# Kernel tuning notes

Hardware: AMD Instinct MI355X
Metric: run time of the kernel (lower is better)

## Reference

```python
import jax, jax.numpy as jnp
import numpy as np

NUM_CLASSES = 10
NUM_NODES = 4096
BATCH = 2048
T_TRAIN = 2048
WDIM = 64
GAMMA = 1.0
ADJ_P = 0.02  # edge density


def setup_inputs() -> dict:
    key = jax.random.key(0)
    ks = jax.random.split(key, 7)
    pred = jax.random.normal(ks[0], (BATCH, NUM_CLASSES), dtype=jnp.float32)
    target = jax.random.randint(ks[1], (BATCH,), 0, NUM_CLASSES, dtype=jnp.int32)
    mask_idx = jnp.arange(BATCH, dtype=jnp.int32)  # nodes selected by boolean `mask`
    adj = jax.random.bernoulli(ks[2], ADJ_P, (NUM_NODES, NUM_NODES))  # bool adjacency
    gem = jax.random.normal(ks[3], (NUM_NODES, T_TRAIN), dtype=jnp.float32)  # global_effect_matrix[:, train_mask]
    w_sub = jax.random.uniform(ks[4], (WDIM, T_TRAIN), dtype=jnp.float32)
    w_inter = jax.random.uniform(ks[5], (WDIM, T_TRAIN), dtype=jnp.float32)
    w_global = jax.random.uniform(ks[6], (WDIM, T_TRAIN), dtype=jnp.float32)
    return dict(pred=pred, gem=gem, w_sub=w_sub, w_inter=w_inter,
                w_global=w_global, adj=adj, target=target, mask_idx=mask_idx)


def reference(pred, gem, w_sub, w_inter, w_global, adj, target, mask_idx):
    B = pred.shape[0]
    dt = pred.dtype
    # linear_*(gem).sum(-1) == gem @ W.sum(0)
    g_sub = gem @ w_sub.sum(axis=0)      # [Nn]
    g_inter = gem @ w_inter.sum(axis=0)  # [Nn]
    g_global = gem @ w_global.sum(axis=0)  # computed in original (vg_i) but unused by loss

    A = adj[mask_idx].astype(dt)                    # [B, Nn] rows of adj for batch nodes
    # adj_self = adj with the diagonal forced True; only gathered rows needed
    As = A.at[jnp.arange(B), mask_idx].set(1.0)     # [B, Nn]

    # vi_sub[p,n] = sum_k (A[p,k] & ~As[n,k]) * g_sub[k]   (dense form of sparse-COO coalesce-sum)
    vi_sub = (A * g_sub) @ (1.0 - As).T             # [B, B]
    # vi_inter[p,n] = sum_k (A[p,k] & A[n,k]) * g_inter[k]
    vi_inter = (A * g_inter) @ A.T                  # [B, B]
    v = 1.0 - jax.nn.sigmoid((1.0 + vi_sub) / (1.0 + vi_inter))  # v_i = 1 - vl_i

    # pairwise SqGAUC kernel: for pair (p,n), class i = target[p]:
    #   d = gamma - (pred[p,i] - pred[n,i]);  K = d^2
    s = jnp.take_along_axis(pred, target[:, None].astype(jnp.int32), axis=1)[:, 0]  # pred[p, t_p]
    cross = jnp.take(pred, target, axis=1).T        # [p, n] = pred[n, t_p]
    d = GAMMA - (s[:, None] - cross)
    K = d * d

    counts = jnp.zeros((NUM_CLASSES,), dt).at[target].add(1.0)  # N per class
    invN = 1.0 / counts[target]                      # 1/N[target[b]]
    pair = (target[:, None] != target[None, :]).astype(dt)      # only i != j pairs
    loss = jnp.sum(pair * (invN[:, None] * invN[None, :]) * v * K)
    return loss.reshape(1)
```

## Files before the change

### kernel.cpp

```cpp
#include <hip/hip_runtime.h>
#include <stdint.h>

#define BATCH 2048
#define NNODE 4096
#define TDIM  2048
#define NCLS  10
#define WDIM  64
#define LCAP  256
#define LPAD  288
#define DEGMAX 128
#define SDUMP 2112
#define FPS   1024.f
#define FPSI  (1.f / 1024.f)

typedef unsigned short u16;
typedef unsigned int   u32;

#define NFILL ((((NNODE + 1) * (DEGMAX / 2)) + 255) / 256)
#define NDEG  (((NNODE + 1) + 255) / 256)

__global__ void k_wsum(const float* __restrict__ w_sub, const float* __restrict__ w_inter,
                       float* __restrict__ wsum_sub, float* __restrict__ wsum_inter,
                       u32* __restrict__ nbrT32, int* __restrict__ degT) {
  int bid = blockIdx.x, tid = threadIdx.x;
  if (bid < 8) {
    int k = bid * 256 + tid;
    float a = 0.f, b = 0.f;
    for (int w = 0; w < WDIM; ++w) {
      a += w_sub[w * TDIM + k];
      b += w_inter[w * TDIM + k];
    }
    wsum_sub[k] = a; wsum_inter[k] = b;
  } else if (bid < 8 + NFILL) {
    int idx = (bid - 8) * 256 + tid;
    if (idx < (NNODE + 1) * (DEGMAX / 2)) {
      int w = idx & 63;
      u32 lo = 2048u + (u32)((2 * w) & 63);
      u32 hi = 2048u + (u32)((2 * w + 1) & 63);
      nbrT32[idx] = lo | (hi << 16);
    }
  } else {
    int idx = (bid - 8 - NFILL) * 256 + tid;
    if (idx < NNODE + 1) degT[idx] = 0;
  }
}

__global__ __launch_bounds__(256) void k_pack(
    const int* __restrict__ adj, const int* __restrict__ mask_idx,
    const float* __restrict__ gem, const float* __restrict__ wsum_sub,
    const float* __restrict__ wsum_inter,
    u32* __restrict__ Adjb, int* __restrict__ diag01,
    u16* __restrict__ nbrT, int* __restrict__ degT,
    float* __restrict__ g_sub, float* __restrict__ g_inter) {
  int bid = blockIdx.x, tid = threadIdx.x;
  if (bid < 2048) {
    int nt = bid >> 6, kt = bid & 63;
    int nl = tid >> 2, kg = tid & 3;
    int n = nt * 64 + nl;
    int row = mask_idx[n];
    const uint4* src = (const uint4*)(adj + (size_t)row * NNODE + kt * 64 + kg * 16);
    uint4 v0 = src[0], v1 = src[1], v2 = src[2], v3 = src[3];
    unsigned m16 = 0;
    m16 |= (unsigned)(v0.x != 0u) << 0;  m16 |= (unsigned)(v0.y != 0u) << 1;
    m16 |= (unsigned)(v0.z != 0u) << 2;  m16 |= (unsigned)(v0.w != 0u) << 3;
    m16 |= (unsigned)(v1.x != 0u) << 4;  m16 |= (unsigned)(v1.y != 0u) << 5;
    m16 |= (unsigned)(v1.z != 0u) << 6;  m16 |= (unsigned)(v1.w != 0u) << 7;
    m16 |= (unsigned)(v2.x != 0u) << 8;  m16 |= (unsigned)(v2.y != 0u) << 9;
    m16 |= (unsigned)(v2.z != 0u) << 10; m16 |= (unsigned)(v2.w != 0u) << 11;
    m16 |= (unsigned)(v3.x != 0u) << 12; m16 |= (unsigned)(v3.y != 0u) << 13;
    m16 |= (unsigned)(v3.z != 0u) << 14; m16 |= (unsigned)(v3.w != 0u) << 15;
    unsigned other = (unsigned)__shfl((int)m16, (tid & 63) ^ 1, 64);
    if ((kg & 1) == 0)
      Adjb[n * 128 + kt * 2 + (kg >> 1)] = m16 | (other << 16);
    if ((row >> 4) == (kt * 4 + kg))
      diag01[n] = (int)((m16 >> (row & 15)) & 1u);
    unsigned r = m16;
    int kb = kt * 64 + kg * 16;
    while (r) {
      int j = __ffs(r) - 1; r &= r - 1;
      int k = kb + j;
      int pos = atomicAdd(&degT[k], 1);
      if (pos < DEGMAX) nbrT[k * DEGMAX + pos] = (u16)n;
    }
  } else {
    int b2 = bid - 2048;
    int wid = tid >> 6, lane = tid & 63;
    int n = b2 * 4 + wid;
    const float4* rowv = (const float4*)(gem + (size_t)n * TDIM);
    const float4* ws4 = (const float4*)wsum_sub;
    const float4* wi4 = (const float4*)wsum_inter;
    float a = 0.f, b = 0.f;
    #pragma unroll
    for (int s = 0; s < TDIM / 256; ++s) {
      int idx = s * 64 + lane;
      float4 g = rowv[idx], u = ws4[idx], v = wi4[idx];
      a += g.x * u.x + g.y * u.y + g.z * u.z + g.w * u.w;
      b += g.x * v.x + g.y * v.y + g.z * v.z + g.w * v.w;
    }
    #pragma unroll
    for (int off = 32; off > 0; off >>= 1) {
      a += __shfl_down(a, off, 64);
      b += __shfl_down(b, off, 64);
    }
    if (lane == 0) { g_sub[n] = a; g_inter[n] = b; }
  }
}

__global__ __launch_bounds__(1024) void k_misc(
    const float* __restrict__ pred, const int* __restrict__ target,
    const int* __restrict__ mask_idx, const int* __restrict__ diag01,
    const float* __restrict__ g_sub,
    float* __restrict__ invN, float* __restrict__ svec,
    float* __restrict__ cvec, float* __restrict__ predT) {
  __shared__ int cnt[NCLS];
  int tid = threadIdx.x, lane = tid & 63;
  if (tid < NCLS) cnt[tid] = 0;
  __syncthreads();
  #pragma unroll
  for (int i = 0; i < BATCH / 1024; ++i) {
    int t = target[tid + i * 1024];
    #pragma unroll
    for (int c = 0; c < NCLS; ++c) {
      unsigned long long m = __ballot(t == c);
      if (lane == 0 && m) atomicAdd(&cnt[c], __popcll(m));
    }
  }
  __syncthreads();
  int nl = tid & 255, cg = tid >> 8;
  int n = blockIdx.x * 256 + nl;
  int t = target[n];
  for (int c = cg; c < NCLS; c += 4)
    predT[c * BATCH + n] = pred[n * NCLS + c];
  if (cg == 0) {
    invN[n] = 1.f / (float)cnt[t];
    svec[n] = pred[n * NCLS + t];
    cvec[n] = diag01[n] ? 0.f : g_sub[mask_idx[n]];
  }
}

__global__ __launch_bounds__(256) void k_main(
    const u32* __restrict__ Adjb, const u16* __restrict__ nbrT,
    const int* __restrict__ degT, const int* __restrict__ target,
    const float* __restrict__ g_sub, const float* __restrict__ g_inter,
    const float* __restrict__ cvec, const float* __restrict__ invN,
    const float* __restrict__ svec, const float* __restrict__ predT,
    const int* __restrict__ mask_idx, float* __restrict__ partial) {
  __shared__ __align__(16) int S1i[SDUMP];
  __shared__ __align__(16) int S2i[SDUMP];
  __shared__ u16 abit[256];
  __shared__ __align__(16) u16 list_s[LPAD];
  __shared__ __align__(16) int2 gpairI[LPAD];
  __shared__ int wcnt[4];
  __shared__ float wred[4];
  __shared__ float rowsum_sh;

  int tid = threadIdx.x, p = blockIdx.x;
  int lane = tid & 63, wid = tid >> 6;

  u32 w = 0;
  if (tid < 128) {
    w = Adjb[p * 128 + tid];
    abit[2 * tid]     = (u16)(w & 0xFFFFu);
    abit[2 * tid + 1] = (u16)(w >> 16);
  }
  int4 zi4 = make_int4(0, 0, 0, 0);
  #pragma unroll
  for (int i = 0; i < 3; ++i) {
    int idx = tid + i * 256;
    if (idx < SDUMP / 4) { ((int4*)S1i)[idx] = zi4; ((int4*)S2i)[idx] = zi4; }
  }
  int cnt = __popc(w);
  int incl = cnt;
  #pragma unroll
  for (int d = 1; d < 64; d <<= 1) {
    int y = __shfl_up(incl, d, 64);
    if (lane >= d) incl += y;
  }
  if (lane == 63) wcnt[wid] = incl;
  __syncthreads();
  int wbase = 0;
  #pragma unroll
  for (int ww = 0; ww < 4; ++ww) if (ww < wid) wbase += wcnt[ww];
  int off = wbase + incl - cnt;
  u32 r = w; int kb = tid * 32;
  while (r) {
    int j = __ffs(r) - 1; r &= r - 1;
    if (off < LCAP) list_s[off] = (u16)(kb + j);
    ++off;
  }
  int total = wcnt[0] + wcnt[1] + wcnt[2] + wcnt[3];
  if (total > LCAP) total = LCAP;
  int totalPad = (total + 3) & ~3;
  __syncthreads();

  float rl = 0.f;
  for (int i = tid; i < LPAD; i += 256) {
    int2 gi2 = make_int2(0, 0);
    if (i < total) {
      int k = list_s[i];
      float gs = g_sub[k], gi = g_inter[k];
      rl += gs;
      gi2.x = (int)rintf(gs * FPS);
      gi2.y = (int)rintf(gi * FPS);
    } else {
      list_s[i] = (u16)NNODE;
    }
    gpairI[i] = gi2;
  }
  #pragma unroll
  for (int o = 32; o > 0; o >>= 1) rl += __shfl_down(rl, o, 64);
  if (lane == 0) wred[wid] = rl;
  __syncthreads();
  if (tid == 0) rowsum_sh = wred[0] + wred[1] + wred[2] + wred[3];

  {
    int nsteps = totalPad >> 2;
    int kc = list_s[wid];
    u16 ec = nbrT[kc * DEGMAX + lane];
    int dc = degT[kc];
    for (int t = 0; t < nsteps; ++t) {
      int inx = (t + 1) * 4 + wid;
      int kn = list_s[inx];
      u16 en = nbrT[kn * DEGMAX + lane];
      int dn = degT[kn];
      int2 g = gpairI[t * 4 + wid];
      atomicAdd(&S1i[ec], g.x);
      atomicAdd(&S2i[ec], g.y);
      if (dc > 64) {
        u16 e2 = nbrT[kc * DEGMAX + 64 + lane];
        atomicAdd(&S1i[e2], g.x);
        atomicAdd(&S2i[e2], g.y);
      }
      kc = kn; ec = en; dc = dn;
    }
  }
  __syncthreads();

  int tp = target[p];
  float sp = svec[p], ip = invN[p], rs = rowsum_sh;
  int n0 = tid * 8;
  int tn[8], mn[8], s1i[8], s2i[8];
  float iN[8], cv[8], pr[8];
  *(int4*)(tn)       = *(const int4*)&target[n0];
  *(int4*)(tn + 4)   = *(const int4*)&target[n0 + 4];
  *(int4*)(mn)       = *(const int4*)&mask_idx[n0];
  *(int4*)(mn + 4)   = *(const int4*)&mask_idx[n0 + 4];
  *(float4*)(iN)     = *(const float4*)&invN[n0];
  *(float4*)(iN + 4) = *(const float4*)&invN[n0 + 4];
  *(float4*)(cv)     = *(const float4*)&cvec[n0];
  *(float4*)(cv + 4) = *(const float4*)&cvec[n0 + 4];
  *(float4*)(pr)     = *(const float4*)&predT[tp * BATCH + n0];
  *(float4*)(pr + 4) = *(const float4*)&predT[tp * BATCH + n0 + 4];
  *(int4*)(s1i)      = *(const int4*)&S1i[n0];
  *(int4*)(s1i + 4)  = *(const int4*)&S1i[n0 + 4];
  *(int4*)(s2i)      = *(const int4*)&S2i[n0];
  *(int4*)(s2i + 4)  = *(const int4*)&S2i[n0 + 4];
  float acc = 0.f;
  #pragma unroll
  for (int j = 0; j < 8; ++j) {
    if (tn[j] == tp) continue;
    float s1 = (float)s1i[j] * FPSI;
    float s2 = (float)s2i[j] * FPSI;
    float apn = ((abit[mn[j] >> 4] >> (mn[j] & 15)) & 1) ? 1.f : 0.f;
    float vs = rs - s1 - apn * cv[j];
    float rr = (1.f + vs) * __builtin_amdgcn_rcpf(1.f + s2);
    float v = __builtin_amdgcn_rcpf(1.f + __expf(rr));
    float d = 1.f - (sp - pr[j]);
    acc += ip * iN[j] * v * d * d;
  }
  #pragma unroll
  for (int o = 32; o > 0; o >>= 1) acc += __shfl_down(acc, o, 64);
  if (lane == 0) wred[wid] = acc;
  __syncthreads();
  if (tid == 0) partial[p] = wred[0] + wred[1] + wred[2] + wred[3];
}

__global__ void k_final(const float* __restrict__ partial, float* __restrict__ out) {
  int tid = threadIdx.x;
  float local = 0.f;
  for (int p = tid; p < BATCH; p += 256) local += partial[p];
  __shared__ float red[4];
  #pragma unroll
  for (int off = 32; off > 0; off >>= 1) local += __shfl_down(local, off, 64);
  if ((tid & 63) == 0) red[tid >> 6] = local;
  __syncthreads();
  if (tid == 0) out[0] = red[0] + red[1] + red[2] + red[3];
}

extern "C" void kernel_launch(void* const* d_in, const int* in_sizes, int n_in,
                              void* d_out, int out_size, void* d_ws, size_t ws_size,
                              hipStream_t stream) {
  const float* pred    = (const float*)d_in[0];
  const float* gem     = (const float*)d_in[1];
  const float* w_sub   = (const float*)d_in[2];
  const float* w_inter = (const float*)d_in[3];
  const int* adj       = (const int*)d_in[5];
  const int* target    = (const int*)d_in[6];
  const int* mask_idx  = (const int*)d_in[7];
  float* out = (float*)d_out;

  char* ws = (char*)d_ws;
  size_t off = 0;
  auto alloc = [&](size_t bytes) {
    void* p = ws + off;
    off = (off + bytes + 255) & ~(size_t)255;
    return p;
  };
  u32*   Adjb     = (u32*)alloc((size_t)BATCH * 128 * 4);
  u16*   nbrT     = (u16*)alloc((size_t)(NNODE + 1) * DEGMAX * 2);
  int*   degT     = (int*)alloc((size_t)(NNODE + 1) * 4);
  int*   diag01   = (int*)alloc((size_t)BATCH * 4);
  float* predT    = (float*)alloc((size_t)NCLS * BATCH * 4);
  float* g_sub    = (float*)alloc((size_t)NNODE * 4);
  float* g_inter  = (float*)alloc((size_t)NNODE * 4);
  float* wsum_sub = (float*)alloc((size_t)TDIM * 4);
  float* wsum_inter=(float*)alloc((size_t)TDIM * 4);
  float* cvec     = (float*)alloc((size_t)BATCH * 4);
  float* invN     = (float*)alloc((size_t)BATCH * 4);
  float* svec     = (float*)alloc((size_t)BATCH * 4);
  float* partial  = (float*)alloc((size_t)BATCH * 4);

  k_wsum<<<8 + NFILL + NDEG, 256, 0, stream>>>(w_sub, w_inter, wsum_sub, wsum_inter,
                                               (u32*)nbrT, degT);
  k_pack<<<2048 + NNODE / 4, 256, 0, stream>>>(adj, mask_idx, gem, wsum_sub, wsum_inter,
                                               Adjb, diag01, nbrT, degT, g_sub, g_inter);
  k_misc<<<BATCH / 256, 1024, 0, stream>>>(pred, target, mask_idx, diag01, g_sub,
                                           invN, svec, cvec, predT);
  k_main<<<BATCH, 256, 0, stream>>>(Adjb, nbrT, degT, target, g_sub, g_inter,
                                    cvec, invN, svec, predT, mask_idx, partial);
  k_final<<<1, 256, 0, stream>>>(partial, out);
}
```

Baseline: 58.74 us.

## Eliminate misc and final kernels by folding into wsum and main

Class counting and invN are now computed in an extra block of the first kernel, and the per-pair cvec, svec and predT values are read directly from pred, g_sub and diag01 inside the main kernel. The final reduction kernel is replaced by an atomicAdd of each block's partial into the output, which the first kernel zeroes. This removes two kernel launches and their dependency gaps. In exchange the main kernel does strided, uncoalesced gathers from pred and g_sub, and float atomics make the summation order nondeterministic.

```diff
diff --git a/kernel.cpp b/kernel.cpp
--- a/kernel.cpp
+++ b/kernel.cpp
@@ -20,10 +20,13 @@
 #define NDEG  (((NNODE + 1) + 255) / 256)
 
 __global__ void k_wsum(const float* __restrict__ w_sub, const float* __restrict__ w_inter,
+                       const int* __restrict__ target,
                        float* __restrict__ wsum_sub, float* __restrict__ wsum_inter,
-                       u32* __restrict__ nbrT32, int* __restrict__ degT) {
+                       u32* __restrict__ nbrT32, int* __restrict__ degT,
+                       float* __restrict__ invN, float* __restrict__ out) {
   int bid = blockIdx.x, tid = threadIdx.x;
   if (bid < 8) {
+    if (bid == 0 && tid == 0) out[0] = 0.f;
     int k = bid * 256 + tid;
     float a = 0.f, b = 0.f;
     for (int w = 0; w < WDIM; ++w) {
@@ -39,9 +42,32 @@
       u32 hi = 2048u + (u32)((2 * w + 1) & 63);
       nbrT32[idx] = lo | (hi << 16);
     }
-  } else {
+  } else if (bid < 8 + NFILL + NDEG) {
     int idx = (bid - 8 - NFILL) * 256 + tid;
     if (idx < NNODE + 1) degT[idx] = 0;
+  } else {
+    __shared__ int cnt[NCLS];
+    __shared__ float cinv[NCLS];
+    int lane = tid & 63;
+    if (tid < NCLS) cnt[tid] = 0;
+    __syncthreads();
+    #pragma unroll
+    for (int i = 0; i < BATCH / 256; ++i) {
+      int t = target[i * 256 + tid];
+      #pragma unroll
+      for (int c = 0; c < NCLS; ++c) {
+        unsigned long long m = __ballot(t == c);
+        if (lane == 0 && m) atomicAdd(&cnt[c], __popcll(m));
+      }
+    }
+    __syncthreads();
+    if (tid < NCLS) cinv[tid] = 1.f / (float)cnt[tid];
+    __syncthreads();
+    #pragma unroll
+    for (int i = 0; i < BATCH / 256; ++i) {
+      int n = i * 256 + tid;
+      invN[n] = cinv[target[n]];
+    }
   }
 }
 
@@ -106,45 +132,13 @@
   }
 }
 
-__global__ __launch_bounds__(1024) void k_misc(
-    const float* __restrict__ pred, const int* __restrict__ target,
-    const int* __restrict__ mask_idx, const int* __restrict__ diag01,
-    const float* __restrict__ g_sub,
-    float* __restrict__ invN, float* __restrict__ svec,
-    float* __restrict__ cvec, float* __restrict__ predT) {
-  __shared__ int cnt[NCLS];
-  int tid = threadIdx.x, lane = tid & 63;
-  if (tid < NCLS) cnt[tid] = 0;
-  __syncthreads();
-  #pragma unroll
-  for (int i = 0; i < BATCH / 1024; ++i) {
-    int t = target[tid + i * 1024];
-    #pragma unroll
-    for (int c = 0; c < NCLS; ++c) {
-      unsigned long long m = __ballot(t == c);
-      if (lane == 0 && m) atomicAdd(&cnt[c], __popcll(m));
-    }
-  }
-  __syncthreads();
-  int nl = tid & 255, cg = tid >> 8;
-  int n = blockIdx.x * 256 + nl;
-  int t = target[n];
-  for (int c = cg; c < NCLS; c += 4)
-    predT[c * BATCH + n] = pred[n * NCLS + c];
-  if (cg == 0) {
-    invN[n] = 1.f / (float)cnt[t];
-    svec[n] = pred[n * NCLS + t];
-    cvec[n] = diag01[n] ? 0.f : g_sub[mask_idx[n]];
-  }
-}
-
 __global__ __launch_bounds__(256) void k_main(
     const u32* __restrict__ Adjb, const u16* __restrict__ nbrT,
     const int* __restrict__ degT, const int* __restrict__ target,
     const float* __restrict__ g_sub, const float* __restrict__ g_inter,
-    const float* __restrict__ cvec, const float* __restrict__ invN,
-    const float* __restrict__ svec, const float* __restrict__ predT,
-    const int* __restrict__ mask_idx, float* __restrict__ partial) {
+    const int* __restrict__ diag01, const float* __restrict__ invN,
+    const float* __restrict__ pred, const int* __restrict__ mask_idx,
+    float* __restrict__ out) {
   __shared__ __align__(16) int S1i[SDUMP];
   __shared__ __align__(16) int S2i[SDUMP];
   __shared__ u16 abit[256];
@@ -237,20 +231,19 @@
   __syncthreads();
 
   int tp = target[p];
-  float sp = svec[p], ip = invN[p], rs = rowsum_sh;
+  float sp = pred[p * NCLS + tp];
+  float ip = invN[p], rs = rowsum_sh;
   int n0 = tid * 8;
-  int tn[8], mn[8], s1i[8], s2i[8];
-  float iN[8], cv[8], pr[8];
+  int tn[8], mn[8], dg[8], s1i[8], s2i[8];
+  float iN[8];
   *(int4*)(tn)       = *(const int4*)&target[n0];
   *(int4*)(tn + 4)   = *(const int4*)&target[n0 + 4];
   *(int4*)(mn)       = *(const int4*)&mask_idx[n0];
   *(int4*)(mn + 4)   = *(const int4*)&mask_idx[n0 + 4];
+  *(int4*)(dg)       = *(const int4*)&diag01[n0];
+  *(int4*)(dg + 4)   = *(const int4*)&diag01[n0 + 4];
   *(float4*)(iN)     = *(const float4*)&invN[n0];
   *(float4*)(iN + 4) = *(const float4*)&invN[n0 + 4];
-  *(float4*)(cv)     = *(const float4*)&cvec[n0];
-  *(float4*)(cv + 4) = *(const float4*)&cvec[n0 + 4];
-  *(float4*)(pr)     = *(const float4*)&predT[tp * BATCH + n0];
-  *(float4*)(pr + 4) = *(const float4*)&predT[tp * BATCH + n0 + 4];
   *(int4*)(s1i)      = *(const int4*)&S1i[n0];
   *(int4*)(s1i + 4)  = *(const int4*)&S1i[n0 + 4];
   *(int4*)(s2i)      = *(const int4*)&S2i[n0];
@@ -259,32 +252,23 @@
   #pragma unroll
   for (int j = 0; j < 8; ++j) {
     if (tn[j] == tp) continue;
+    float cv = dg[j] ? 0.f : g_sub[mn[j]];
+    float pr = pred[(n0 + j) * NCLS + tp];
     float s1 = (float)s1i[j] * FPSI;
     float s2 = (float)s2i[j] * FPSI;
     float apn = ((abit[mn[j] >> 4] >> (mn[j] & 15)) & 1) ? 1.f : 0.f;
-    float vs = rs - s1 - apn * cv[j];
+    float vs = rs - s1 - apn * cv;
     float rr = (1.f + vs) * __builtin_amdgcn_rcpf(1.f + s2);
     float v = __builtin_amdgcn_rcpf(1.f + __expf(rr));
-    float d = 1.f - (sp - pr[j]);
+    float d = 1.f - (sp - pr);
     acc += ip * iN[j] * v * d * d;
   }
   #pragma unroll
   for (int o = 32; o > 0; o >>= 1) acc += __shfl_down(acc, o, 64);
   if (lane == 0) wred[wid] = acc;
   __syncthreads();
-  if (tid == 0) partial[p] = wred[0] + wred[1] + wred[2] + wred[3];
-}
-
-__global__ void k_final(const float* __restrict__ partial, float* __restrict__ out) {
-  int tid = threadIdx.x;
-  float local = 0.f;
-  for (int p = tid; p < BATCH; p += 256) local += partial[p];
-  __shared__ float red[4];
-  #pragma unroll
-  for (int off = 32; off > 0; off >>= 1) local += __shfl_down(local, off, 64);
-  if ((tid & 63) == 0) red[tid >> 6] = local;
-  __syncthreads();
-  if (tid == 0) out[0] = red[0] + red[1] + red[2] + red[3];
+  if (tid == 0)
+    atomicAdd(out, wred[0] + wred[1] + wred[2] + wred[3]);
 }
 
 extern "C" void kernel_launch(void* const* d_in, const int* in_sizes, int n_in,
@@ -310,23 +294,17 @@
   u16*   nbrT     = (u16*)alloc((size_t)(NNODE + 1) * DEGMAX * 2);
   int*   degT     = (int*)alloc((size_t)(NNODE + 1) * 4);
   int*   diag01   = (int*)alloc((size_t)BATCH * 4);
-  float* predT    = (float*)alloc((size_t)NCLS * BATCH * 4);
   float* g_sub    = (float*)alloc((size_t)NNODE * 4);
   float* g_inter  = (float*)alloc((size_t)NNODE * 4);
   float* wsum_sub = (float*)alloc((size_t)TDIM * 4);
   float* wsum_inter=(float*)alloc((size_t)TDIM * 4);
-  float* cvec     = (float*)alloc((size_t)BATCH * 4);
   float* invN     = (float*)alloc((size_t)BATCH * 4);
-  float* svec     = (float*)alloc((size_t)BATCH * 4);
-  float* partial  = (float*)alloc((size_t)BATCH * 4);
-
-  k_wsum<<<8 + NFILL + NDEG, 256, 0, stream>>>(w_sub, w_inter, wsum_sub, wsum_inter,
-                                               (u32*)nbrT, degT);
+
+  k_wsum<<<8 + NFILL + NDEG + 1, 256, 0, stream>>>(w_sub, w_inter, target,
+                                                   wsum_sub, wsum_inter,
+                                                   (u32*)nbrT, degT, invN, out);
   k_pack<<<2048 + NNODE / 4, 256, 0, stream>>>(adj, mask_idx, gem, wsum_sub, wsum_inter,
                                                Adjb, diag01, nbrT, degT, g_sub, g_inter);
-  k_misc<<<BATCH / 256, 1024, 0, stream>>>(pred, target, mask_idx, diag01, g_sub,
-                                           invN, svec, cvec, predT);
   k_main<<<BATCH, 256, 0, stream>>>(Adjb, nbrT, degT, target, g_sub, g_inter,
-                                    cvec, invN, svec, predT, mask_idx, partial);
-  k_final<<<1, 256, 0, stream>>>(partial, out);
+                                    diag01, invN, pred, mask_idx, out);
 }
```

After: 73.84 us. +25.7%, slower.
